# Kernel tuning notes

Measured on AMD Instinct MI355X. Metric: run time of the kernel, lower is better.

## Reference

```python
import jax, jax.numpy as jnp
import numpy as np

N = 6144
IN_DIM = 256
OUT_DIM = 256
NUM_HEADS = 4
HEAD_DIM = OUT_DIM // NUM_HEADS  # 64
NEG_SLOPE = 0.2


def setup_inputs() -> dict:
    key = jax.random.key(0)
    k_x, k_adj, k_W, k_a = jax.random.split(key, 4)
    x = jax.random.normal(k_x, (N, IN_DIM), dtype=jnp.float32)
    adj = jax.random.randint(k_adj, (N, N), 0, 2, dtype=jnp.int32)
    # nn.Linear(in_dim, out_dim, bias=False): store as [in_dim, out_dim] so y = x @ W
    W = jax.random.normal(k_W, (IN_DIM, OUT_DIM), dtype=jnp.float32) / np.sqrt(IN_DIM)
    # nn.Linear(2*head_dim, 1, bias=False): a single attention vector shared across heads
    a = jax.random.normal(k_a, (2 * HEAD_DIM,), dtype=jnp.float32) / np.sqrt(2 * HEAD_DIM)
    return {"x": x, "adj": adj, "W": W, "a": a}


def reference(x, adj, W, a):
    n = x.shape[0]
    Wh = (x @ W).reshape(n, NUM_HEADS, HEAD_DIM)  # (N, H, D)
    a_src, a_dst = a[:HEAD_DIM], a[HEAD_DIM:]
    # score[h,i,j] = leaky_relu(a_src . Wh[i,h] + a_dst . Wh[j,h])
    f_src = jnp.einsum('nhd,d->hn', Wh, a_src)  # (H, N)
    f_dst = jnp.einsum('nhd,d->hn', Wh, a_dst)  # (H, N)
    e = f_src[:, :, None] + f_dst[:, None, :]   # (H, N, N)
    e = jnp.where(e > 0, e, NEG_SLOPE * e)      # LeakyReLU(0.2)
    mask = (adj != 0)[None, :, :]               # (1, N, N)
    e = jnp.where(mask, e, -jnp.inf)
    alpha = jax.nn.softmax(e, axis=-1)          # (H, N, N)
    alpha = jnp.nan_to_num(alpha, nan=0.0)      # empty rows -> 0 (matches torch)
    # dropout: eval mode (identity)
    out = jnp.einsum('hij,jhd->ihd', alpha, Wh).reshape(n, OUT_DIM)
    return out
```

## Files before the change

kernel.cpp:

```cpp
#include <hip/hip_runtime.h>

#define NN 6144
#define SHIFTC (12.0f*1.4426950408889634f)
#define LOG2E 1.4426950408889634f

typedef float f32x4 __attribute__((ext_vector_type(4)));
typedef short short8 __attribute__((ext_vector_type(8)));
typedef int   i32x4 __attribute__((ext_vector_type(4)));

__device__ __forceinline__ float bf2f(unsigned short u){
  return __uint_as_float(((unsigned int)u)<<16);
}
__device__ __forceinline__ unsigned short f2bf(float f){
  unsigned int x = __float_as_uint(f);
  x += 0x7fffu + ((x>>16)&1u);
  return (unsigned short)(x>>16);
}

__global__ __launch_bounds__(256) void k_gemm(const float* __restrict__ x,
                                              const float* __restrict__ W,
                                              unsigned short* __restrict__ wht){
  __shared__ float sx[16*256];
  const int t = threadIdx.x;
  const int i0 = blockIdx.x * 16;
  {
    const int r = t >> 4, kc = t & 15;
    const float* src = x + (size_t)(i0 + r)*256 + kc*16;
    float* dst = sx + r*256 + kc*16;
#pragma unroll
    for (int q = 0; q < 4; ++q)
      *reinterpret_cast<f32x4*>(dst + 4*q) = *reinterpret_cast<const f32x4*>(src + 4*q);
  }
  __syncthreads();
  float acc[16];
#pragma unroll
  for (int r = 0; r < 16; ++r) acc[r] = 0.f;
  for (int k = 0; k < 256; k += 4) {
    const float w0 = W[(size_t)(k+0)*256 + t];
    const float w1 = W[(size_t)(k+1)*256 + t];
    const float w2 = W[(size_t)(k+2)*256 + t];
    const float w3 = W[(size_t)(k+3)*256 + t];
#pragma unroll
    for (int r = 0; r < 16; ++r) {
      f32x4 xv = *reinterpret_cast<const f32x4*>(sx + r*256 + k);
      acc[r] = fmaf(xv.x, w0, acc[r]);
      acc[r] = fmaf(xv.y, w1, acc[r]);
      acc[r] = fmaf(xv.z, w2, acc[r]);
      acc[r] = fmaf(xv.w, w3, acc[r]);
    }
  }
  alignas(16) unsigned short buf[16];
#pragma unroll
  for (int r = 0; r < 16; ++r) buf[r] = f2bf(acc[r]);
  unsigned short* dst = wht + (size_t)t*NN + i0;
  *reinterpret_cast<uint4*>(dst)     = *reinterpret_cast<const uint4*>(buf);
  *reinterpret_cast<uint4*>(dst + 8) = *reinterpret_cast<const uint4*>(buf + 8);
}

__global__ __launch_bounds__(256) void k_f(const unsigned short* __restrict__ wht,
                                           const float* __restrict__ a,
                                           float* __restrict__ fs2,
                                           float* __restrict__ edp,
                                           float* __restrict__ edn){
  __shared__ unsigned short sw[256*64];
  const int t = threadIdx.x;
  const int i0 = blockIdx.x * 64;
  {
    const unsigned short* src = wht + (size_t)t*NN + i0;
    unsigned short* dst = sw + t*64;
#pragma unroll
    for (int q = 0; q < 8; ++q)
      *reinterpret_cast<uint4*>(dst + q*8) = *reinterpret_cast<const uint4*>(src + q*8);
  }
  __syncthreads();
  const int ii = t & 63, h = t >> 6;
  float s_ = 0.f, d_ = 0.f;
#pragma unroll 16
  for (int d = 0; d < 64; ++d) {
    const float v = bf2f(sw[(h*64 + d)*64 + ii]);
    s_ = fmaf(v, a[d],      s_);
    d_ = fmaf(v, a[64 + d], d_);
  }
  const float fs2v = s_ * LOG2E;
  const float fd2v = d_ * LOG2E;
  fs2[(size_t)h*NN + i0 + ii] = fs2v;
  edp[(size_t)h*NN + i0 + ii] = exp2f(fd2v - SHIFTC);
  edn[(size_t)h*NN + i0 + ii] = exp2f(0.2f * fd2v);
}

__global__ __launch_bounds__(256) void k_attn(const int* __restrict__ adj,
                                              const unsigned short* __restrict__ wht,
                                              const float* __restrict__ fs2,
                                              const float* __restrict__ edp,
                                              const float* __restrict__ edn,
                                              float* __restrict__ apart,
                                              float* __restrict__ lpart,
                                              int nsteps){
  __shared__ unsigned short swht[256*72];
  __shared__ unsigned int   smask[64*2];
  __shared__ float          sedp[256];
  __shared__ float          sedn[256];
  const int t  = threadIdx.x;
  const int w  = t >> 6, l = t & 63, lr = l & 15, hi = l >> 4;
  const int it = blockIdx.x % 96;
  const int js = blockIdx.x / 96;
  const int i0 = it * 64;
  const int jbase = js * nsteps * 64;
  const int i_row = i0 + w*16 + lr;

  float TP[4], EiN[4];
#pragma unroll
  for (int h = 0; h < 4; ++h) {
    const float f = fs2[(size_t)h*NN + i_row];
    TP[h]  = exp2f(-f - SHIFTC);
    EiN[h] = exp2f(-0.8f*f - SHIFTC);
  }
  f32x4 acc[16];
#pragma unroll
  for (int q = 0; q < 16; ++q) acc[q] = (f32x4){0.f,0.f,0.f,0.f};
  float ls[4] = {0.f,0.f,0.f,0.f};

  const int r_ = t >> 2, ch_ = t & 3;
  const int* asrc = adj + (size_t)(i0 + r_)*NN + jbase + ch_*16;

  i32x4 ajp[4];
#pragma unroll
  for (int q = 0; q < 4; ++q)
    ajp[q] = *reinterpret_cast<const i32x4*>(asrc + q*4);

  for (int st = 0; st < nsteps; ++st) {
    const int j0 = jbase + st*64;
    __syncthreads();
    {
      const unsigned short* src = wht + (size_t)t*NN + j0;
      unsigned short* dst = swht + t*72;
#pragma unroll
      for (int q = 0; q < 8; ++q)
        *reinterpret_cast<uint4*>(dst + q*8) = *reinterpret_cast<const uint4*>(src + q*8);
    }
    {
      unsigned int bits = 0u;
#pragma unroll
      for (int q = 0; q < 4; ++q) {
        bits |= (ajp[q].x != 0 ? 1u : 0u) << (q*4 + 0);
        bits |= (ajp[q].y != 0 ? 1u : 0u) << (q*4 + 1);
        bits |= (ajp[q].z != 0 ? 1u : 0u) << (q*4 + 2);
        bits |= (ajp[q].w != 0 ? 1u : 0u) << (q*4 + 3);
      }
      reinterpret_cast<unsigned short*>(smask)[r_*4 + ch_] = (unsigned short)bits;
    }
    {
      sedp[t] = edp[(size_t)(t >> 6)*NN + j0 + (t & 63)];
      sedn[t] = edn[(size_t)(t >> 6)*NN + j0 + (t & 63)];
    }
    __syncthreads();

    if (st + 1 < nsteps) {
      const int* an = asrc + (st + 1)*64;
#pragma unroll
      for (int q = 0; q < 4; ++q)
        ajp[q] = *reinterpret_cast<const i32x4*>(an + q*4);
    }

    const unsigned int m0 = smask[(w*16 + lr)*2 + 0];
    const unsigned int m1 = smask[(w*16 + lr)*2 + 1];
    float maskf[16];
#pragma unroll
    for (int e = 0; e < 8; ++e) {
      maskf[e]     = ((m0 >> (8*hi + e)) & 1u) ? 1.f : 0.f;
      maskf[8 + e] = ((m1 >> (8*hi + e)) & 1u) ? 1.f : 0.f;
    }
#pragma unroll
    for (int h = 0; h < 4; ++h) {
      const float TPh = TP[h], EiNh = EiN[h];
      const f32x4 ep0 = *reinterpret_cast<const f32x4*>(&sedp[h*64 + 8*hi + 0]);
      const f32x4 ep1 = *reinterpret_cast<const f32x4*>(&sedp[h*64 + 8*hi + 4]);
      const f32x4 ep2 = *reinterpret_cast<const f32x4*>(&sedp[h*64 + 32 + 8*hi + 0]);
      const f32x4 ep3 = *reinterpret_cast<const f32x4*>(&sedp[h*64 + 32 + 8*hi + 4]);
      const f32x4 en0 = *reinterpret_cast<const f32x4*>(&sedn[h*64 + 8*hi + 0]);
      const f32x4 en1 = *reinterpret_cast<const f32x4*>(&sedn[h*64 + 8*hi + 4]);
      const f32x4 en2 = *reinterpret_cast<const f32x4*>(&sedn[h*64 + 32 + 8*hi + 0]);
      const f32x4 en3 = *reinterpret_cast<const f32x4*>(&sedn[h*64 + 32 + 8*hi + 4]);
      float p[16];
#pragma unroll
      for (int e = 0; e < 4; ++e) {
        p[e]      = maskf[e]      * (ep0[e] > TPh ? ep0[e] : EiNh * en0[e]);
        p[4 + e]  = maskf[4 + e]  * (ep1[e] > TPh ? ep1[e] : EiNh * en1[e]);
        p[8 + e]  = maskf[8 + e]  * (ep2[e] > TPh ? ep2[e] : EiNh * en2[e]);
        p[12 + e] = maskf[12 + e] * (ep3[e] > TPh ? ep3[e] : EiNh * en3[e]);
      }
      float lsh = 0.f;
#pragma unroll
      for (int e = 0; e < 16; ++e) lsh += p[e];
      ls[h] += lsh;
      int4 aw0, aw1;
      asm("v_cvt_pk_bf16_f32 %0, %1, %2" : "=v"(aw0.x) : "v"(p[0]),  "v"(p[1]));
      asm("v_cvt_pk_bf16_f32 %0, %1, %2" : "=v"(aw0.y) : "v"(p[2]),  "v"(p[3]));
      asm("v_cvt_pk_bf16_f32 %0, %1, %2" : "=v"(aw0.z) : "v"(p[4]),  "v"(p[5]));
      asm("v_cvt_pk_bf16_f32 %0, %1, %2" : "=v"(aw0.w) : "v"(p[6]),  "v"(p[7]));
      asm("v_cvt_pk_bf16_f32 %0, %1, %2" : "=v"(aw1.x) : "v"(p[8]),  "v"(p[9]));
      asm("v_cvt_pk_bf16_f32 %0, %1, %2" : "=v"(aw1.y) : "v"(p[10]), "v"(p[11]));
      asm("v_cvt_pk_bf16_f32 %0, %1, %2" : "=v"(aw1.z) : "v"(p[12]), "v"(p[13]));
      asm("v_cvt_pk_bf16_f32 %0, %1, %2" : "=v"(aw1.w) : "v"(p[14]), "v"(p[15]));
      const short8 af0 = __builtin_bit_cast(short8, aw0);
      const short8 af1 = __builtin_bit_cast(short8, aw1);
#pragma unroll
      for (int nc = 0; nc < 4; ++nc) {
        const unsigned short* bp = swht + (size_t)(h*64 + nc*16 + lr)*72 + 8*hi;
        const short8 b0 = *reinterpret_cast<const short8*>(bp);
        const short8 b1 = *reinterpret_cast<const short8*>(bp + 32);
        acc[h*4 + nc] = __builtin_amdgcn_mfma_f32_16x16x32_bf16(af0, b0, acc[h*4 + nc], 0, 0, 0);
        acc[h*4 + nc] = __builtin_amdgcn_mfma_f32_16x16x32_bf16(af1, b1, acc[h*4 + nc], 0, 0, 0);
      }
    }
  }

#pragma unroll
  for (int h = 0; h < 4; ++h) {
    float v = ls[h];
    v += __shfl_xor(v, 16, 64);
    v += __shfl_xor(v, 32, 64);
    ls[h] = v;
  }
  if (hi == 0) {
#pragma unroll
    for (int h = 0; h < 4; ++h)
      lpart[((size_t)js*4 + h)*NN + i_row] = ls[h];
  }
#pragma unroll
  for (int h = 0; h < 4; ++h)
#pragma unroll
    for (int nc = 0; nc < 4; ++nc)
#pragma unroll
      for (int rg = 0; rg < 4; ++rg) {
        const int irow = i0 + w*16 + 4*hi + rg;
        const int col  = h*64 + nc*16 + lr;
        apart[((size_t)js*NN + irow)*256 + col] = acc[h*4 + nc][rg];
      }
}

__global__ __launch_bounds__(256) void k_comb(const float* __restrict__ apart,
                                              const float* __restrict__ lpart,
                                              float* __restrict__ out,
                                              int jsplit){
  const int idx = blockIdx.x * 256 + threadIdx.x;
  const int i = idx >> 8, c = idx & 255, h = c >> 6;
  float num = 0.f, den = 0.f;
  for (int s = 0; s < jsplit; ++s) {
    num += apart[((size_t)s*NN + i)*256 + c];
    den += lpart[((size_t)s*4 + h)*NN + i];
  }
  out[idx] = (den > 0.f) ? (num / den) : 0.f;
}

extern "C" void kernel_launch(void* const* d_in, const int* in_sizes, int n_in,
                              void* d_out, int out_size, void* d_ws, size_t ws_size,
                              hipStream_t stream) {
  const float* x   = (const float*)d_in[0];
  const int*   adj = (const int*)d_in[1];
  const float* W   = (const float*)d_in[2];
  const float* a   = (const float*)d_in[3];
  float* out = (float*)d_out;
  char* ws = (char*)d_ws;

  size_t off = 0;
  unsigned short* wht = (unsigned short*)(ws + off); off += (size_t)256*NN*2;
  float* fs2 = (float*)(ws + off); off += (size_t)4*NN*4;
  float* edp = (float*)(ws + off); off += (size_t)4*NN*4;
  float* edn = (float*)(ws + off); off += (size_t)4*NN*4;

  int jsplit = 8;
  while (jsplit > 1 &&
         off + (size_t)jsplit*4*NN*4 + (size_t)jsplit*NN*256*4 > ws_size)
    jsplit >>= 1;

  float* lpart = (float*)(ws + off); off += (size_t)jsplit*4*NN*4;
  float* apart = (float*)(ws + off);

  const int nsteps = NN / (jsplit * 64);

  k_gemm<<<dim3(NN/16), dim3(256), 0, stream>>>(x, W, wht);
  k_f   <<<dim3(NN/64), dim3(256), 0, stream>>>(wht, a, fs2, edp, edn);
  k_attn<<<dim3((NN/64)*jsplit), dim3(256), 0, stream>>>(adj, wht, fs2, edp, edn, apart, lpart, nsteps);
  k_comb<<<dim3((out_size + 255)/256), dim3(256), 0, stream>>>(apart, lpart, out, jsplit);
}
```

Baseline: 138.6 us.

## Split attention kernel across heads, one head per block

Each attention block now handles a single head instead of all four, and the grid grows four-fold. The head index and tile index are packed into the block ID so that the four blocks for the same rows and j-range launch close together, which should let them share adj reads through L2. Per-block shared memory, accumulator registers and per-step work each drop by a factor of four, aiming at higher occupancy and more parallelism. The cost is that every block reads the adjacency mask itself, so each adj tile is loaded four times, and the mask conversion is repeated per head.

```diff
diff --git a/kernel.cpp b/kernel.cpp
--- a/kernel.cpp
+++ b/kernel.cpp
@@ -96,32 +96,33 @@
                                               float* __restrict__ apart,
                                               float* __restrict__ lpart,
                                               int nsteps){
-  __shared__ unsigned short swht[256*72];
+  __shared__ unsigned short swht[64*72];
   __shared__ unsigned int   smask[64*2];
-  __shared__ float          sedp[256];
-  __shared__ float          sedn[256];
+  __shared__ float          sedp[64];
+  __shared__ float          sedn[64];
   const int t  = threadIdx.x;
   const int w  = t >> 6, l = t & 63, lr = l & 15, hi = l >> 4;
-  const int it = blockIdx.x % 96;
-  const int js = blockIdx.x / 96;
+  const int bid = blockIdx.x;
+  const int h   = (bid >> 3) & 3;
+  const int g   = (bid & 7) | ((bid >> 5) << 3);
+  const int it  = g % 96;
+  const int js  = g / 96;
   const int i0 = it * 64;
   const int jbase = js * nsteps * 64;
   const int i_row = i0 + w*16 + lr;
 
-  float TP[4], EiN[4];
-#pragma unroll
-  for (int h = 0; h < 4; ++h) {
-    const float f = fs2[(size_t)h*NN + i_row];
-    TP[h]  = exp2f(-f - SHIFTC);
-    EiN[h] = exp2f(-0.8f*f - SHIFTC);
-  }
-  f32x4 acc[16];
-#pragma unroll
-  for (int q = 0; q < 16; ++q) acc[q] = (f32x4){0.f,0.f,0.f,0.f};
-  float ls[4] = {0.f,0.f,0.f,0.f};
+  const float fsv  = fs2[(size_t)h*NN + i_row];
+  const float TPh  = exp2f(-fsv - SHIFTC);
+  const float EiNh = exp2f(-0.8f*fsv - SHIFTC);
+
+  f32x4 acc[4];
+#pragma unroll
+  for (int q = 0; q < 4; ++q) acc[q] = (f32x4){0.f,0.f,0.f,0.f};
+  float ls = 0.f;
 
   const int r_ = t >> 2, ch_ = t & 3;
   const int* asrc = adj + (size_t)(i0 + r_)*NN + jbase + ch_*16;
+  const unsigned short* wsrc = wht + (size_t)(h*64 + r_)*NN + jbase + ch_*16;
 
   i32x4 ajp[4];
 #pragma unroll
@@ -132,11 +133,10 @@
     const int j0 = jbase + st*64;
     __syncthreads();
     {
-      const unsigned short* src = wht + (size_t)t*NN + j0;
-      unsigned short* dst = swht + t*72;
-#pragma unroll
-      for (int q = 0; q < 8; ++q)
-        *reinterpret_cast<uint4*>(dst + q*8) = *reinterpret_cast<const uint4*>(src + q*8);
+      const unsigned short* src = wsrc + st*64;
+      unsigned short* dst = swht + r_*72 + ch_*16;
+      *reinterpret_cast<uint4*>(dst)     = *reinterpret_cast<const uint4*>(src);
+      *reinterpret_cast<uint4*>(dst + 8) = *reinterpret_cast<const uint4*>(src + 8);
     }
     {
       unsigned int bits = 0u;
@@ -149,9 +149,9 @@
       }
       reinterpret_cast<unsigned short*>(smask)[r_*4 + ch_] = (unsigned short)bits;
     }
-    {
-      sedp[t] = edp[(size_t)(t >> 6)*NN + j0 + (t & 63)];
-      sedn[t] = edn[(size_t)(t >> 6)*NN + j0 + (t & 63)];
+    if (t < 64) {
+      sedp[t] = edp[(size_t)h*NN + j0 + t];
+      sedn[t] = edn[(size_t)h*NN + j0 + t];
     }
     __syncthreads();
 
@@ -170,73 +170,63 @@
       maskf[e]     = ((m0 >> (8*hi + e)) & 1u) ? 1.f : 0.f;
       maskf[8 + e] = ((m1 >> (8*hi + e)) & 1u) ? 1.f : 0.f;
     }
-#pragma unroll
-    for (int h = 0; h < 4; ++h) {
-      const float TPh = TP[h], EiNh = EiN[h];
-      const f32x4 ep0 = *reinterpret_cast<const f32x4*>(&sedp[h*64 + 8*hi + 0]);
-      const f32x4 ep1 = *reinterpret_cast<const f32x4*>(&sedp[h*64 + 8*hi + 4]);
-      const f32x4 ep2 = *reinterpret_cast<const f32x4*>(&sedp[h*64 + 32 + 8*hi + 0]);
-      const f32x4 ep3 = *reinterpret_cast<const f32x4*>(&sedp[h*64 + 32 + 8*hi + 4]);
-      const f32x4 en0 = *reinterpret_cast<const f32x4*>(&sedn[h*64 + 8*hi + 0]);
-      const f32x4 en1 = *reinterpret_cast<const f32x4*>(&sedn[h*64 + 8*hi + 4]);
-      const f32x4 en2 = *reinterpret_cast<const f32x4*>(&sedn[h*64 + 32 + 8*hi + 0]);
-      const f32x4 en3 = *reinterpret_cast<const f32x4*>(&sedn[h*64 + 32 + 8*hi + 4]);
-      float p[16];
-#pragma unroll
-      for (int e = 0; e < 4; ++e) {
-        p[e]      = maskf[e]      * (ep0[e] > TPh ? ep0[e] : EiNh * en0[e]);
-        p[4 + e]  = maskf[4 + e]  * (ep1[e] > TPh ? ep1[e] : EiNh * en1[e]);
-        p[8 + e]  = maskf[8 + e]  * (ep2[e] > TPh ? ep2[e] : EiNh * en2[e]);
-        p[12 + e] = maskf[12 + e] * (ep3[e] > TPh ? ep3[e] : EiNh * en3[e]);
-      }
-      float lsh = 0.f;
-#pragma unroll
-      for (int e = 0; e < 16; ++e) lsh += p[e];
-      ls[h] += lsh;
-      int4 aw0, aw1;
-      asm("v_cvt_pk_bf16_f32 %0, %1, %2" : "=v"(aw0.x) : "v"(p[0]),  "v"(p[1]));
-      asm("v_cvt_pk_bf16_f32 %0, %1, %2" : "=v"(aw0.y) : "v"(p[2]),  "v"(p[3]));
-      asm("v_cvt_pk_bf16_f32 %0, %1, %2" : "=v"(aw0.z) : "v"(p[4]),  "v"(p[5]));
-      asm("v_cvt_pk_bf16_f32 %0, %1, %2" : "=v"(aw0.w) : "v"(p[6]),  "v"(p[7]));
-      asm("v_cvt_pk_bf16_f32 %0, %1, %2" : "=v"(aw1.x) : "v"(p[8]),  "v"(p[9]));
-      asm("v_cvt_pk_bf16_f32 %0, %1, %2" : "=v"(aw1.y) : "v"(p[10]), "v"(p[11]));
-      asm("v_cvt_pk_bf16_f32 %0, %1, %2" : "=v"(aw1.z) : "v"(p[12]), "v"(p[13]));
-      asm("v_cvt_pk_bf16_f32 %0, %1, %2" : "=v"(aw1.w) : "v"(p[14]), "v"(p[15]));
-      const short8 af0 = __builtin_bit_cast(short8, aw0);
-      const short8 af1 = __builtin_bit_cast(short8, aw1);
-#pragma unroll
-      for (int nc = 0; nc < 4; ++nc) {
-        const unsigned short* bp = swht + (size_t)(h*64 + nc*16 + lr)*72 + 8*hi;
-        const short8 b0 = *reinterpret_cast<const short8*>(bp);
-        const short8 b1 = *reinterpret_cast<const short8*>(bp + 32);
-        acc[h*4 + nc] = __builtin_amdgcn_mfma_f32_16x16x32_bf16(af0, b0, acc[h*4 + nc], 0, 0, 0);
-        acc[h*4 + nc] = __builtin_amdgcn_mfma_f32_16x16x32_bf16(af1, b1, acc[h*4 + nc], 0, 0, 0);
-      }
-    }
-  }
-
-#pragma unroll
-  for (int h = 0; h < 4; ++h) {
-    float v = ls[h];
+    const f32x4 ep0 = *reinterpret_cast<const f32x4*>(&sedp[8*hi + 0]);
+    const f32x4 ep1 = *reinterpret_cast<const f32x4*>(&sedp[8*hi + 4]);
+    const f32x4 ep2 = *reinterpret_cast<const f32x4*>(&sedp[32 + 8*hi + 0]);
+    const f32x4 ep3 = *reinterpret_cast<const f32x4*>(&sedp[32 + 8*hi + 4]);
+    const f32x4 en0 = *reinterpret_cast<const f32x4*>(&sedn[8*hi + 0]);
+    const f32x4 en1 = *reinterpret_cast<const f32x4*>(&sedn[8*hi + 4]);
+    const f32x4 en2 = *reinterpret_cast<const f32x4*>(&sedn[32 + 8*hi + 0]);
+    const f32x4 en3 = *reinterpret_cast<const f32x4*>(&sedn[32 + 8*hi + 4]);
+    float p[16];
+#pragma unroll
+    for (int e = 0; e < 4; ++e) {
+      p[e]      = maskf[e]      * (ep0[e] > TPh ? ep0[e] : EiNh * en0[e]);
+      p[4 + e]  = maskf[4 + e]  * (ep1[e] > TPh ? ep1[e] : EiNh * en1[e]);
+      p[8 + e]  = maskf[8 + e]  * (ep2[e] > TPh ? ep2[e] : EiNh * en2[e]);
+      p[12 + e] = maskf[12 + e] * (ep3[e] > TPh ? ep3[e] : EiNh * en3[e]);
+    }
+    float lsh = 0.f;
+#pragma unroll
+    for (int e = 0; e < 16; ++e) lsh += p[e];
+    ls += lsh;
+    int4 aw0, aw1;
+    asm("v_cvt_pk_bf16_f32 %0, %1, %2" : "=v"(aw0.x) : "v"(p[0]),  "v"(p[1]));
+    asm("v_cvt_pk_bf16_f32 %0, %1, %2" : "=v"(aw0.y) : "v"(p[2]),  "v"(p[3]));
+    asm("v_cvt_pk_bf16_f32 %0, %1, %2" : "=v"(aw0.z) : "v"(p[4]),  "v"(p[5]));
+    asm("v_cvt_pk_bf16_f32 %0, %1, %2" : "=v"(aw0.w) : "v"(p[6]),  "v"(p[7]));
+    asm("v_cvt_pk_bf16_f32 %0, %1, %2" : "=v"(aw1.x) : "v"(p[8]),  "v"(p[9]));
+    asm("v_cvt_pk_bf16_f32 %0, %1, %2" : "=v"(aw1.y) : "v"(p[10]), "v"(p[11]));
+    asm("v_cvt_pk_bf16_f32 %0, %1, %2" : "=v"(aw1.z) : "v"(p[12]), "v"(p[13]));
+    asm("v_cvt_pk_bf16_f32 %0, %1, %2" : "=v"(aw1.w) : "v"(p[14]), "v"(p[15]));
+    const short8 af0 = __builtin_bit_cast(short8, aw0);
+    const short8 af1 = __builtin_bit_cast(short8, aw1);
+#pragma unroll
+    for (int nc = 0; nc < 4; ++nc) {
+      const unsigned short* bp = swht + (size_t)(nc*16 + lr)*72 + 8*hi;
+      const short8 b0 = *reinterpret_cast<const short8*>(bp);
+      const short8 b1 = *reinterpret_cast<const short8*>(bp + 32);
+      acc[nc] = __builtin_amdgcn_mfma_f32_16x16x32_bf16(af0, b0, acc[nc], 0, 0, 0);
+      acc[nc] = __builtin_amdgcn_mfma_f32_16x16x32_bf16(af1, b1, acc[nc], 0, 0, 0);
+    }
+  }
+
+  {
+    float v = ls;
     v += __shfl_xor(v, 16, 64);
     v += __shfl_xor(v, 32, 64);
-    ls[h] = v;
-  }
-  if (hi == 0) {
-#pragma unroll
-    for (int h = 0; h < 4; ++h)
-      lpart[((size_t)js*4 + h)*NN + i_row] = ls[h];
-  }
-#pragma unroll
-  for (int h = 0; h < 4; ++h)
-#pragma unroll
-    for (int nc = 0; nc < 4; ++nc)
-#pragma unroll
-      for (int rg = 0; rg < 4; ++rg) {
-        const int irow = i0 + w*16 + 4*hi + rg;
-        const int col  = h*64 + nc*16 + lr;
-        apart[((size_t)js*NN + irow)*256 + col] = acc[h*4 + nc][rg];
-      }
+    ls = v;
+  }
+  if (hi == 0)
+    lpart[((size_t)js*4 + h)*NN + i_row] = ls;
+#pragma unroll
+  for (int nc = 0; nc < 4; ++nc)
+#pragma unroll
+    for (int rg = 0; rg < 4; ++rg) {
+      const int irow = i0 + w*16 + 4*hi + rg;
+      const int col  = h*64 + nc*16 + lr;
+      apart[((size_t)js*NN + irow)*256 + col] = acc[nc][rg];
+    }
 }
 
 __global__ __launch_bounds__(256) void k_comb(const float* __restrict__ apart,
@@ -281,6 +271,6 @@
 
   k_gemm<<<dim3(NN/16), dim3(256), 0, stream>>>(x, W, wht);
   k_f   <<<dim3(NN/64), dim3(256), 0, stream>>>(wht, a, fs2, edp, edn);
-  k_attn<<<dim3((NN/64)*jsplit), dim3(256), 0, stream>>>(adj, wht, fs2, edp, edn, apart, lpart, nsteps);
+  k_attn<<<dim3(4*(NN/64)*jsplit), dim3(256), 0, stream>>>(adj, wht, fs2, edp, edn, apart, lpart, nsteps);
   k_comb<<<dim3((out_size + 255)/256), dim3(256), 0, stream>>>(apart, lpart, out, jsplit);
 }
```

New measurement: 121.7 us. -12.2%, faster.
